# Optimization experiments

Measured on AMD Instinct MI355X. Metric: run time of the kernel, lower is better.

## Reference

```python
import jax, jax.numpy as jnp
import numpy as np

M, NQ, NKV = 8, 256, 4096
E, H, D = 1024, 16, 64  # embed_dim, num_heads, head_dim
SCALE = D ** -0.5


def setup_inputs() -> dict:
    key = jax.random.key(0)
    ks = jax.random.split(key, 6)
    zq = jax.random.normal(ks[0], (M, NQ, E), dtype=jnp.float32)
    zkv = jax.random.normal(ks[1], (M, NKV, E), dtype=jnp.float32)
    xq = jax.random.normal(ks[2], (M, NQ, E), dtype=jnp.float32)
    xkv = jax.random.normal(ks[3], (M, NKV, E), dtype=jnp.float32)
    Wq = jax.random.normal(ks[4], (E, H * D), dtype=jnp.float32) / np.sqrt(E)
    Wk = jax.random.normal(ks[5], (E, H * D), dtype=jnp.float32) / np.sqrt(E)
    raw_head_weights = jnp.ones((H,), dtype=jnp.float32)
    return {"zq": zq, "zkv": zkv, "xq": xq, "xkv": xkv,
            "Wq": Wq, "Wk": Wk, "raw_head_weights": raw_head_weights}


def reference(zq, zkv, xq, xkv, Wq, Wk, raw_head_weights):
    # project + split heads: [m, h, n, d]
    q = jnp.einsum('mne,ehd->mhnd', zq, Wq.reshape(E, H, D))
    k = jnp.einsum('mne,ehd->mhnd', zkv, Wk.reshape(E, H, D))
    # SDPA with V = xkv broadcast across heads
    scores = jnp.einsum('mhqd,mhkd->mhqk', q, k) * SCALE
    attn = jax.nn.softmax(scores, axis=-1)
    # attn @ V with broadcast V [m, nkv, dx] -> per-head outputs [m, h, nq, dx]
    out = jnp.einsum('mhqk,mkd->mhqd', attn, xkv)
    # head-weighted combine + residual
    head_weights = jax.nn.softmax(raw_head_weights, axis=0)
    xq_update = jnp.einsum('mhqd,h->mqd', out, head_weights)
    xq_out = xq + xq_update
    return (zq, xq_out)
```

## Files before the change

kernel.cpp:

```cpp
#include <hip/hip_runtime.h>
#include <hip/hip_bf16.h>
#include <stdint.h>

#define MB_  8
#define NQ_  256
#define NKV_ 4096
#define E_   1024
#define H_   16
#define D_   64

typedef __bf16 bf16x8 __attribute__((ext_vector_type(8)));
typedef float  f32x4  __attribute__((ext_vector_type(4)));
typedef unsigned short u16;
typedef unsigned short u16x8 __attribute__((ext_vector_type(8)));

#define MFMA16(a,b,c) __builtin_amdgcn_mfma_f32_16x16x32_bf16((a),(b),(c),0,0,0)

__device__ __forceinline__ u16 f2bf(float f) {
  uint32_t u = __float_as_uint(f);
  u += 0x7fffu + ((u >> 16) & 1u);
  return (u16)(u >> 16);
}

__device__ __forceinline__ void gload_lds16(const void* g, void* l) {
  __builtin_amdgcn_global_load_lds(
      (const __attribute__((address_space(1))) void*)g,
      (__attribute__((address_space(3))) void*)l, 16, 0, 0);
}

__device__ __forceinline__ void stage_tile(const char* __restrict__ g, int ldbytes,
                                           char* lds, int t) {
  int srcCB = (((t & 7) ^ ((t >> 3) & 7)) << 4);
  const char* gp = g + (long long)(t >> 3) * ldbytes + srcCB;
  char* lp = lds + ((t >> 6) << 10);
#pragma unroll
  for (int i = 0; i < 4; ++i) {
    gload_lds16(gp + (long long)(32 * i) * ldbytes, lp + i * 4096);
  }
}

__device__ __forceinline__ bf16x8 read_frag(const char* lds, int r, int cb) {
  return *(const bf16x8*)(lds + r * 128 + (cb ^ ((r & 7) << 4)));
}

template <int MODE>
__global__ __launch_bounds__(256, 2) void gemm_nt(
    const u16* __restrict__ A, const u16* __restrict__ Bt, void* __restrict__ Cv,
    int lda, int ldb, int ldc, int K,
    long long sA, long long sB, long long sC) {
  __shared__ __align__(16) char smA[16384];
  __shared__ __align__(16) char smB[16384];
  int zz = blockIdx.z;
  int b = (MODE == 2) ? (zz & 7) : zz;
  int ks = (MODE == 2) ? (zz >> 3) : 0;
  long long koff = (long long)ks * 1024;

  unsigned nwg = gridDim.x * gridDim.y;
  unsigned orig = blockIdx.y * gridDim.x + blockIdx.x;
  unsigned cpx = nwg >> 3;
  unsigned swz = (orig & 7) * cpx + (orig >> 3);
  unsigned bx = swz % gridDim.x, by = swz / gridDim.x;

  const char* Ap = (const char*)(A + (long long)b * sA + (long long)by * 128 * lda + koff);
  const char* Bp = (const char*)(Bt + (long long)b * sB + (long long)bx * 128 * ldb + koff);

  int t = threadIdx.x, lane = t & 63;
  int wm = t >> 7, wn = (t >> 6) & 1;
  int rl = lane & 15, kq = lane >> 4;

  f32x4 acc[4][4];
#pragma unroll
  for (int i = 0; i < 4; ++i)
#pragma unroll
    for (int j = 0; j < 4; ++j) acc[i][j] = (f32x4){0.f, 0.f, 0.f, 0.f};

  int ldab = lda * 2, ldbb = ldb * 2;
  for (int k0 = 0; k0 < K; k0 += 64) {
    stage_tile(Ap + k0 * 2, ldab, smA, t);
    stage_tile(Bp + k0 * 2, ldbb, smB, t);
    __syncthreads();
    bf16x8 af[4][2], bf[4][2];
#pragma unroll
    for (int f = 0; f < 4; ++f)
#pragma unroll
      for (int ksl = 0; ksl < 2; ++ksl) {
        af[f][ksl] = read_frag(smA, wm * 64 + f * 16 + rl, ksl * 64 + kq * 16);
        bf[f][ksl] = read_frag(smB, wn * 64 + f * 16 + rl, ksl * 64 + kq * 16);
      }
#pragma unroll
    for (int fm = 0; fm < 4; ++fm)
#pragma unroll
      for (int fn = 0; fn < 4; ++fn) {
        acc[fm][fn] = MFMA16(af[fm][0], bf[fn][0], acc[fm][fn]);
        acc[fm][fn] = MFMA16(af[fm][1], bf[fn][1], acc[fm][fn]);
      }
    __syncthreads();
  }

#pragma unroll
  for (int fm = 0; fm < 4; ++fm)
#pragma unroll
    for (int fn = 0; fn < 4; ++fn)
#pragma unroll
      for (int j = 0; j < 4; ++j) {
        int row = by * 128 + wm * 64 + fm * 16 + kq * 4 + j;
        int col = bx * 128 + wn * 64 + fn * 16 + rl;
        if (MODE == 0) {
          ((u16*)Cv)[(long long)b * sC + (long long)row * ldc + col] = f2bf(acc[fm][fn][j]);
        } else {
          ((float*)Cv)[((long long)(ks * 8 + b)) * sC + (long long)row * ldc + col] =
              acc[fm][fn][j];
        }
      }
}

__device__ __forceinline__ void stage32(const char* __restrict__ g, int ldbytes,
                                        char* ldsbuf, int t, long long koffB) {
  int w = t >> 6, lane = t & 63;
#pragma unroll
  for (int i = 0; i < 2; ++i) {
    int c = w + i * 8;
    int slot = c * 64 + lane;
    int row = slot >> 2, c16 = slot & 3;
    int srcc = (c16 ^ ((row >> 1) & 3)) << 4;
    gload_lds16(g + (long long)row * ldbytes + koffB + srcc,
                ldsbuf + c * 1024);
  }
}

__device__ __forceinline__ bf16x8 frag32(const char* ldsbuf, int r, int kq) {
  return *(const bf16x8*)(ldsbuf + r * 64 + ((kq ^ ((r >> 1) & 3)) << 4));
}

__global__ __launch_bounds__(512, 2) void gemm256(
    const u16* __restrict__ A, const u16* __restrict__ Bt, u16* __restrict__ C,
    int lda, int ldb, int ldc, int K) {
  extern __shared__ char lds[];

  unsigned nwg = gridDim.x * gridDim.y;
  unsigned orig = blockIdx.y * gridDim.x + blockIdx.x;
  unsigned cpx = nwg >> 3;
  unsigned swz = (orig & 7) * cpx + (orig >> 3);
  unsigned bx = swz % gridDim.x, by = swz / gridDim.x;

  const char* Ap = (const char*)(A + (long long)by * 256 * lda);
  const char* Bp = (const char*)(Bt + (long long)bx * 256 * ldb);
  int ldab = lda * 2, ldbb = ldb * 2;

  int t = threadIdx.x, lane = t & 63;
  int wid = t >> 6, wm = wid >> 2, wn = wid & 3;
  int rl = lane & 15, kq = lane >> 4;

  f32x4 acc[8][4];
#pragma unroll
  for (int i = 0; i < 8; ++i)
#pragma unroll
    for (int j = 0; j < 4; ++j) acc[i][j] = (f32x4){0.f, 0.f, 0.f, 0.f};

  stage32(Ap, ldab, lds, t, 0);
  stage32(Bp, ldbb, lds + 16384, t, 0);
  stage32(Ap, ldab, lds + 32768, t, 64);
  stage32(Bp, ldbb, lds + 32768 + 16384, t, 64);
  asm volatile("s_waitcnt vmcnt(4)" ::: "memory");
  asm volatile("s_barrier" ::: "memory");

  int NT = K >> 5;
  for (int ts = 0; ts < NT; ++ts) {
    char* bufA = lds + (ts & 3) * 32768;
    char* bufB = bufA + 16384;
    if (ts + 2 < NT) {
      char* nb = lds + ((ts + 2) & 3) * 32768;
      stage32(Ap, ldab, nb, t, (long long)(ts + 2) << 6);
      stage32(Bp, ldbb, nb + 16384, t, (long long)(ts + 2) << 6);
    }
    bf16x8 af[8], bv[4];
#pragma unroll
    for (int fr = 0; fr < 8; ++fr) af[fr] = frag32(bufA, wm * 128 + fr * 16 + rl, kq);
#pragma unroll
    for (int fc = 0; fc < 4; ++fc) bv[fc] = frag32(bufB, wn * 64 + fc * 16 + rl, kq);
    __builtin_amdgcn_s_setprio(1);
#pragma unroll
    for (int fr = 0; fr < 8; ++fr)
#pragma unroll
      for (int fc = 0; fc < 4; ++fc)
        acc[fr][fc] = MFMA16(af[fr], bv[fc], acc[fr][fc]);
    __builtin_amdgcn_s_setprio(0);
    if (ts + 2 < NT)
      asm volatile("s_waitcnt vmcnt(4)" ::: "memory");
    else
      asm volatile("s_waitcnt vmcnt(0)" ::: "memory");
    asm volatile("s_barrier" ::: "memory");
  }

#pragma unroll
  for (int fr = 0; fr < 8; ++fr)
#pragma unroll
    for (int fc = 0; fc < 4; ++fc)
#pragma unroll
      for (int j = 0; j < 4; ++j) {
        int row = by * 256 + wm * 128 + fr * 16 + kq * 4 + j;
        int col = bx * 256 + wn * 64 + fc * 16 + rl;
        C[(long long)row * ldc + col] = f2bf(acc[fr][fc][j]);
      }
}

__global__ void pv_combine_copy(const float* __restrict__ part, const float* __restrict__ xq,
                                const float* __restrict__ zq, float* __restrict__ out0,
                                float* __restrict__ out1) {
  int bid = blockIdx.x;
  if (bid < 2048) {
    int i = bid * 256 + threadIdx.x;
    ((float4*)out0)[i] = ((const float4*)zq)[i];
  } else {
    int i = (bid - 2048) * 256 + threadIdx.x;
    float4 s = ((const float4*)xq)[i];
#pragma unroll
    for (int k = 0; k < 4; ++k) {
      float4 p = ((const float4*)(part + (long long)k * 2097152))[i];
      s.x += p.x; s.y += p.y; s.z += p.z; s.w += p.w;
    }
    ((float4*)out1)[i] = s;
  }
}

__global__ __launch_bounds__(256, 4) void attn_stats(
    const u16* __restrict__ qg, const u16* __restrict__ kg,
    float* __restrict__ lstP) {
  __shared__ __align__(16) char smQ[16384];
  __shared__ __align__(16) char smK[16384];
  int kt = blockIdx.x, qt = blockIdx.y;
  int m = blockIdx.z >> 1, hh = blockIdx.z & 1;
  int t = threadIdx.x, lane = t & 63;
  int wm = t >> 7, wn = (t >> 6) & 1;
  int rl = lane & 15, kq = lane >> 4;

  const char* qbase = (const char*)(qg + ((long long)(m * NQ_ + qt * 128)) * 1024);
  const char* kbase = (const char*)(kg + ((long long)(m * NKV_ + kt * 128)) * 1024);

  for (int hi = 0; hi < 8; ++hi) {
    int h = hh * 8 + hi;
    stage_tile(qbase + h * 128, 2048, smQ, t);
    stage_tile(kbase + h * 128, 2048, smK, t);
    __syncthreads();
    bf16x8 kf[4][2], qf[4][2];
#pragma unroll
    for (int f = 0; f < 4; ++f)
#pragma unroll
      for (int ksl = 0; ksl < 2; ++ksl) {
        kf[f][ksl] = read_frag(smK, wm * 64 + f * 16 + rl, ksl * 64 + kq * 16);
        qf[f][ksl] = read_frag(smQ, wn * 64 + f * 16 + rl, ksl * 64 + kq * 16);
      }
    float rs[4] = {0.f, 0.f, 0.f, 0.f};
#pragma unroll
    for (int fm = 0; fm < 4; ++fm)
#pragma unroll
      for (int fn = 0; fn < 4; ++fn) {
        f32x4 sc = (f32x4){0.f, 0.f, 0.f, 0.f};
        sc = MFMA16(kf[fm][0], qf[fn][0], sc);
        sc = MFMA16(kf[fm][1], qf[fn][1], sc);
        rs[fn] += (__expf(sc[0]) + __expf(sc[1])) + (__expf(sc[2]) + __expf(sc[3]));
      }
#pragma unroll
    for (int fn = 0; fn < 4; ++fn) {
      float v = rs[fn];
      v += __shfl_xor(v, 16);
      v += __shfl_xor(v, 32);
      if (lane < 16) {
        int q = qt * 128 + wn * 64 + fn * 16 + rl;
        lstP[(long long)(kt * 2 + wm) * 32768 + ((m * H_ + h) << 8) + q] = v;
      }
    }
    __syncthreads();
  }
}

__global__ void stats_combine(const float* __restrict__ lp, float* __restrict__ lst) {
  int i = blockIdx.x * 256 + threadIdx.x;
  float s = 0.f;
#pragma unroll
  for (int k = 0; k < 64; ++k) s += lp[(long long)k * 32768 + i];
  lst[i] = s;
}

__global__ __launch_bounds__(256, 2) void pbar_kernel(
    const u16* __restrict__ qg, const u16* __restrict__ kg,
    const float* __restrict__ lstat,
    const float* __restrict__ rawhw, u16* __restrict__ Pbar) {
  __shared__ __align__(16) char smQ[16384];
  __shared__ __align__(16) char smK[16384];
  __shared__ float scf[2048];
  int kt = blockIdx.x, qt = blockIdx.y, m = blockIdx.z;
  int q0 = qt * 128, k0 = kt * 128;
  int t = threadIdx.x, lane = t & 63;
  int wm = t >> 7, wn = (t >> 6) & 1;
  int rl = lane & 15, kq = lane >> 4;

  float hm = -1e30f;
  for (int i = 0; i < H_; ++i) hm = fmaxf(hm, rawhw[i]);
  float hs = 0.f, hw[H_];
  for (int i = 0; i < H_; ++i) { hw[i] = __expf(rawhw[i] - hm); hs += hw[i]; }
  float hinv = 1.f / hs;
  for (int idx = t; idx < 2048; idx += 256) {
    int h = idx >> 7, r = idx & 127;
    scf[idx] = hw[h] * hinv / lstat[((m * H_ + h) << 8) + q0 + r];
  }

  f32x4 pacc[4][4];
#pragma unroll
  for (int i = 0; i < 4; ++i)
#pragma unroll
    for (int j = 0; j < 4; ++j) pacc[i][j] = (f32x4){0.f, 0.f, 0.f, 0.f};

  const char* qbase = (const char*)(qg + ((long long)(m * NQ_ + q0)) * 1024);
  const char* kbase = (const char*)(kg + ((long long)(m * NKV_ + k0)) * 1024);

  for (int h = 0; h < H_; ++h) {
    stage_tile(qbase + h * 128, 2048, smQ, t);
    stage_tile(kbase + h * 128, 2048, smK, t);
    __syncthreads();
    bf16x8 af[4][2], bfr[4][2];
#pragma unroll
    for (int f = 0; f < 4; ++f)
#pragma unroll
      for (int ksl = 0; ksl < 2; ++ksl) {
        af[f][ksl] = read_frag(smQ, wm * 64 + f * 16 + rl, ksl * 64 + kq * 16);
        bfr[f][ksl] = read_frag(smK, wn * 64 + f * 16 + rl, ksl * 64 + kq * 16);
      }
#pragma unroll
    for (int fm = 0; fm < 4; ++fm) {
      int rbase = wm * 64 + fm * 16 + kq * 4;
      float cf0 = scf[(h << 7) + rbase + 0];
      float cf1 = scf[(h << 7) + rbase + 1];
      float cf2 = scf[(h << 7) + rbase + 2];
      float cf3 = scf[(h << 7) + rbase + 3];
#pragma unroll
      for (int fn = 0; fn < 4; ++fn) {
        f32x4 sc = (f32x4){0.f, 0.f, 0.f, 0.f};
        sc = MFMA16(af[fm][0], bfr[fn][0], sc);
        sc = MFMA16(af[fm][1], bfr[fn][1], sc);
        pacc[fm][fn][0] += cf0 * __expf(sc[0]);
        pacc[fm][fn][1] += cf1 * __expf(sc[1]);
        pacc[fm][fn][2] += cf2 * __expf(sc[2]);
        pacc[fm][fn][3] += cf3 * __expf(sc[3]);
      }
    }
    __syncthreads();
  }
#pragma unroll
  for (int fm = 0; fm < 4; ++fm)
#pragma unroll
    for (int fn = 0; fn < 4; ++fn)
#pragma unroll
      for (int j = 0; j < 4; ++j) {
        int row = q0 + wm * 64 + fm * 16 + kq * 4 + j;
        int col = k0 + wn * 64 + fn * 16 + rl;
        Pbar[(((long long)m * NQ_ + row) << 12) + col] = f2bf(pacc[fm][fn][j]);
      }
}

__global__ void prep_kernel(const float* __restrict__ zq, u16* __restrict__ zqb,
                            const float* __restrict__ zkv, u16* __restrict__ zkvb,
                            const float* __restrict__ Wq, u16* __restrict__ WqT,
                            const float* __restrict__ Wk, u16* __restrict__ WkT,
                            const float* __restrict__ xkv, u16* __restrict__ xkvT) {
  __shared__ float tile[64][65];
  int bid = blockIdx.x;
  if (bid < 17408) {
    const float* in; u16* out; long long i;
    if (bid < 1024) { in = zq; out = zqb; i = (long long)bid * 256 + threadIdx.x; }
    else { in = zkv; out = zkvb; i = (long long)(bid - 1024) * 256 + threadIdx.x; }
    const float4* p = (const float4*)in + i * 2;
    float4 a = p[0], b = p[1];
    u16x8 v;
    v[0] = f2bf(a.x); v[1] = f2bf(a.y); v[2] = f2bf(a.z); v[3] = f2bf(a.w);
    v[4] = f2bf(b.x); v[5] = f2bf(b.y); v[6] = f2bf(b.z); v[7] = f2bf(b.w);
    *(u16x8*)(out + i * 8) = v;
    return;
  }
  const float* in; u16* out; int R, C; float alpha; int r0, c0;
  if (bid < 17664) {
    int id = bid - 17408;
    in = Wq; out = WqT; R = 1024; C = 1024; alpha = 0.125f;
    r0 = (id & 15) * 64; c0 = (id >> 4) * 64;
  } else if (bid < 17920) {
    int id = bid - 17664;
    in = Wk; out = WkT; R = 1024; C = 1024; alpha = 1.0f;
    r0 = (id & 15) * 64; c0 = (id >> 4) * 64;
  } else {
    int id = bid - 17920;
    int bz = id >> 10, rem = id & 1023;
    in = xkv + (long long)bz * NKV_ * E_;
    out = xkvT + (long long)bz * NKV_ * E_;
    R = NKV_; C = E_; alpha = 1.0f;
    r0 = (rem & 63) * 64; c0 = (rem >> 6) * 64;
  }
  int t = threadIdx.x;
  int rr = t >> 4, c4 = t & 15;
#pragma unroll
  for (int i = 0; i < 4; ++i) {
    float4 v = *(const float4*)(in + (long long)(r0 + rr + i * 16) * C + c0 + c4 * 4);
    float* d = &tile[rr + i * 16][c4 * 4];
    d[0] = v.x; d[1] = v.y; d[2] = v.z; d[3] = v.w;
  }
  __syncthreads();
  int cc = t >> 3, r8 = t & 7;
#pragma unroll
  for (int i = 0; i < 2; ++i) {
    int c = cc + i * 32;
    u16x8 v;
#pragma unroll
    for (int j = 0; j < 8; ++j) v[j] = f2bf(alpha * tile[r8 * 8 + j][c]);
    *(u16x8*)(out + (long long)(c0 + c) * R + r0 + r8 * 8) = v;
  }
}

extern "C" void kernel_launch(void* const* d_in, const int* in_sizes, int n_in,
                              void* d_out, int out_size, void* d_ws, size_t ws_size,
                              hipStream_t stream) {
  const float* zq  = (const float*)d_in[0];
  const float* zkv = (const float*)d_in[1];
  const float* xq  = (const float*)d_in[2];
  const float* xkv = (const float*)d_in[3];
  const float* Wq  = (const float*)d_in[4];
  const float* Wk  = (const float*)d_in[5];
  const float* rhw = (const float*)d_in[6];
  float* out = (float*)d_out;

  char* ws = (char*)d_ws;
  u16* WqT  = (u16*)(ws);
  u16* WkT  = (u16*)(ws + (2ull << 20));
  u16* zqb  = (u16*)(ws + (4ull << 20));
  u16* qb   = (u16*)(ws + (8ull << 20));
  u16* kb   = (u16*)(ws + (12ull << 20));
  u16* xkvT = (u16*)(ws + (76ull << 20));
  char* zr  = ws + (140ull << 20);
  u16* zkvb = (u16*)zr;
  u16* Pbar = (u16*)zr;
  float* lst  = (float*)(zr + (18ull << 20));
  float* lstP = (float*)(zr + (20ull << 20));
  float* pvP  = (float*)(zr + (28ull << 20));

  (void)hipFuncSetAttribute((const void*)gemm256,
                            hipFuncAttributeMaxDynamicSharedMemorySize, 131072);

  prep_kernel<<<26112, 256, 0, stream>>>(zq, zqb, zkv, zkvb, Wq, WqT, Wk, WkT, xkv, xkvT);

  gemm_nt<0><<<dim3(8, 16, 1), 256, 0, stream>>>(zqb, WqT, qb,
                                                 1024, 1024, 1024, 1024, 0, 0, 0);
  gemm256<<<dim3(4, 128, 1), 512, 131072, stream>>>(zkvb, WkT, kb, 1024, 1024, 1024, 1024);

  attn_stats<<<dim3(32, 2, 16), 256, 0, stream>>>(qb, kb, lstP);
  stats_combine<<<128, 256, 0, stream>>>(lstP, lst);

  pbar_kernel<<<dim3(32, 2, 8), 256, 0, stream>>>(qb, kb, lst, rhw, Pbar);

  gemm_nt<2><<<dim3(8, 2, 32), 256, 0, stream>>>(Pbar, xkvT, pvP,
                                                 4096, 4096, 1024, 1024,
                                                 256LL * 4096, 1024LL * 4096,
                                                 256LL * 1024);
  pv_combine_copy<<<4096, 256, 0, stream>>>(pvP, xq, zq, out,
                                            out + (long long)MB_ * NQ_ * E_);
}
```

Baseline: 300.9 us.

## Fuse zkv fp32-to-bf16 conversion into the K-projection GEMM A-operand load

The separate prep pass that converted zkv (32768x1024 fp32) to bf16 is removed. The K-projection GEMM now loads fp32 A tiles into registers, converts them to bf16 and writes swizzled LDS itself, with a register double buffer and a 2-stage LDS buffer in place of the 4-stage async-to-LDS pipeline. This drops one full write and reread of the bf16 copy of zkv. In exchange the GEMM reads A at twice the byte width, uses more VGPRs, and runs a shallower pipeline.

```diff
diff --git a/kernel.cpp b/kernel.cpp
--- a/kernel.cpp
+++ b/kernel.cpp
@@ -114,8 +114,8 @@
       }
 }
 
-__device__ __forceinline__ void stage32(const char* __restrict__ g, int ldbytes,
-                                        char* ldsbuf, int t, long long koffB) {
+__device__ __forceinline__ void stageB32(const char* __restrict__ g, int ldbytes,
+                                         char* ldsbuf, int t, long long koffB) {
   int w = t >> 6, lane = t & 63;
 #pragma unroll
   for (int i = 0; i < 2; ++i) {
@@ -123,8 +123,29 @@
     int slot = c * 64 + lane;
     int row = slot >> 2, c16 = slot & 3;
     int srcc = (c16 ^ ((row >> 1) & 3)) << 4;
-    gload_lds16(g + (long long)row * ldbytes + koffB + srcc,
-                ldsbuf + c * 1024);
+    gload_lds16(g + (long long)row * ldbytes + koffB + srcc, ldsbuf + c * 1024);
+  }
+}
+
+__device__ __forceinline__ void loadA32(const float* __restrict__ Apf, int lda,
+                                        int t, int k0, float4 r[4]) {
+  int row = t >> 1, kh = (t & 1) * 16;
+  const float* p = Apf + (long long)row * lda + k0 + kh;
+#pragma unroll
+  for (int i = 0; i < 4; ++i) r[i] = *(const float4*)(p + i * 4);
+}
+
+__device__ __forceinline__ void writeA32(char* bufA, int t, const float4 r[4]) {
+  int row = t >> 1, kh = t & 1;
+  int sw = (row >> 1) & 3;
+#pragma unroll
+  for (int i = 0; i < 2; ++i) {
+    float4 a = r[i * 2], b = r[i * 2 + 1];
+    u16x8 v;
+    v[0] = f2bf(a.x); v[1] = f2bf(a.y); v[2] = f2bf(a.z); v[3] = f2bf(a.w);
+    v[4] = f2bf(b.x); v[5] = f2bf(b.y); v[6] = f2bf(b.z); v[7] = f2bf(b.w);
+    int c16 = kh * 2 + i;
+    *(u16x8*)(bufA + row * 64 + ((c16 ^ sw) << 4)) = v;
   }
 }
 
@@ -132,8 +153,8 @@
   return *(const bf16x8*)(ldsbuf + r * 64 + ((kq ^ ((r >> 1) & 3)) << 4));
 }
 
-__global__ __launch_bounds__(512, 2) void gemm256(
-    const u16* __restrict__ A, const u16* __restrict__ Bt, u16* __restrict__ C,
+__global__ __launch_bounds__(512, 2) void gemm256f(
+    const float* __restrict__ A, const u16* __restrict__ Bt, u16* __restrict__ C,
     int lda, int ldb, int ldc, int K) {
   extern __shared__ char lds[];
 
@@ -143,52 +164,91 @@
   unsigned swz = (orig & 7) * cpx + (orig >> 3);
   unsigned bx = swz % gridDim.x, by = swz / gridDim.x;
 
-  const char* Ap = (const char*)(A + (long long)by * 256 * lda);
+  const float* Apf = A + (long long)by * 256 * lda;
   const char* Bp = (const char*)(Bt + (long long)bx * 256 * ldb);
-  int ldab = lda * 2, ldbb = ldb * 2;
+  int ldbb = ldb * 2;
 
   int t = threadIdx.x, lane = t & 63;
   int wid = t >> 6, wm = wid >> 2, wn = wid & 3;
   int rl = lane & 15, kq = lane >> 4;
 
+  char* bufA0 = lds;
+  char* bufA1 = lds + 16384;
+  char* bufB0 = lds + 32768;
+  char* bufB1 = lds + 49152;
+
   f32x4 acc[8][4];
 #pragma unroll
   for (int i = 0; i < 8; ++i)
 #pragma unroll
     for (int j = 0; j < 4; ++j) acc[i][j] = (f32x4){0.f, 0.f, 0.f, 0.f};
 
-  stage32(Ap, ldab, lds, t, 0);
-  stage32(Bp, ldbb, lds + 16384, t, 0);
-  stage32(Ap, ldab, lds + 32768, t, 64);
-  stage32(Bp, ldbb, lds + 32768 + 16384, t, 64);
-  asm volatile("s_waitcnt vmcnt(4)" ::: "memory");
+  float4 rEven[4], rOdd[4];
+
+  stageB32(Bp, ldbb, bufB0, t, 0);
+  __builtin_amdgcn_sched_barrier(0);
+  loadA32(Apf, lda, t, 0, rEven);
+  loadA32(Apf, lda, t, 32, rOdd);
+  asm volatile("s_waitcnt vmcnt(0)" ::: "memory");
+  writeA32(bufA0, t, rEven);
+  asm volatile("s_waitcnt lgkmcnt(0)" ::: "memory");
   asm volatile("s_barrier" ::: "memory");
 
   int NT = K >> 5;
-  for (int ts = 0; ts < NT; ++ts) {
-    char* bufA = lds + (ts & 3) * 32768;
-    char* bufB = bufA + 16384;
+  for (int ts = 0; ts < NT; ts += 2) {
+    if (ts + 1 < NT) stageB32(Bp, ldbb, bufB1, t, (long long)(ts + 1) << 6);
+    __builtin_amdgcn_sched_barrier(0);
+    if (ts + 2 < NT) loadA32(Apf, lda, t, (ts + 2) << 5, rEven);
+    {
+      bf16x8 af[8], bv[4];
+#pragma unroll
+      for (int fr = 0; fr < 8; ++fr) af[fr] = frag32(bufA0, wm * 128 + fr * 16 + rl, kq);
+#pragma unroll
+      for (int fc = 0; fc < 4; ++fc) bv[fc] = frag32(bufB0, wn * 64 + fc * 16 + rl, kq);
+      __builtin_amdgcn_s_setprio(1);
+#pragma unroll
+      for (int fr = 0; fr < 8; ++fr)
+#pragma unroll
+        for (int fc = 0; fc < 4; ++fc)
+          acc[fr][fc] = MFMA16(af[fr], bv[fc], acc[fr][fc]);
+      __builtin_amdgcn_s_setprio(0);
+    }
+    if (ts + 1 < NT) {
+      if (ts + 2 < NT)
+        asm volatile("s_waitcnt vmcnt(4)" ::: "memory");
+      else
+        asm volatile("s_waitcnt vmcnt(0)" ::: "memory");
+      writeA32(bufA1, t, rOdd);
+      asm volatile("s_waitcnt lgkmcnt(0)" ::: "memory");
+    }
+    asm volatile("s_barrier" ::: "memory");
+    if (ts + 1 >= NT) break;
+
+    if (ts + 2 < NT) stageB32(Bp, ldbb, bufB0, t, (long long)(ts + 2) << 6);
+    __builtin_amdgcn_sched_barrier(0);
+    if (ts + 3 < NT) loadA32(Apf, lda, t, (ts + 3) << 5, rOdd);
+    {
+      bf16x8 af[8], bv[4];
+#pragma unroll
+      for (int fr = 0; fr < 8; ++fr) af[fr] = frag32(bufA1, wm * 128 + fr * 16 + rl, kq);
+#pragma unroll
+      for (int fc = 0; fc < 4; ++fc) bv[fc] = frag32(bufB1, wn * 64 + fc * 16 + rl, kq);
+      __builtin_amdgcn_s_setprio(1);
+#pragma unroll
+      for (int fr = 0; fr < 8; ++fr)
+#pragma unroll
+        for (int fc = 0; fc < 4; ++fc)
+          acc[fr][fc] = MFMA16(af[fr], bv[fc], acc[fr][fc]);
+      __builtin_amdgcn_s_setprio(0);
+    }
     if (ts + 2 < NT) {
-      char* nb = lds + ((ts + 2) & 3) * 32768;
-      stage32(Ap, ldab, nb, t, (long long)(ts + 2) << 6);
-      stage32(Bp, ldbb, nb + 16384, t, (long long)(ts + 2) << 6);
-    }
-    bf16x8 af[8], bv[4];
-#pragma unroll
-    for (int fr = 0; fr < 8; ++fr) af[fr] = frag32(bufA, wm * 128 + fr * 16 + rl, kq);
-#pragma unroll
-    for (int fc = 0; fc < 4; ++fc) bv[fc] = frag32(bufB, wn * 64 + fc * 16 + rl, kq);
-    __builtin_amdgcn_s_setprio(1);
-#pragma unroll
-    for (int fr = 0; fr < 8; ++fr)
-#pragma unroll
-      for (int fc = 0; fc < 4; ++fc)
-        acc[fr][fc] = MFMA16(af[fr], bv[fc], acc[fr][fc]);
-    __builtin_amdgcn_s_setprio(0);
-    if (ts + 2 < NT)
-      asm volatile("s_waitcnt vmcnt(4)" ::: "memory");
-    else
-      asm volatile("s_waitcnt vmcnt(0)" ::: "memory");
+      if (ts + 3 < NT)
+        asm volatile("s_waitcnt vmcnt(4)" ::: "memory");
+      else
+        asm volatile("s_waitcnt vmcnt(0)" ::: "memory");
+      writeA32(bufA0, t, rEven);
+      asm volatile("s_waitcnt lgkmcnt(0)" ::: "memory");
+    }
     asm volatile("s_barrier" ::: "memory");
   }
 
@@ -359,35 +419,32 @@
 }
 
 __global__ void prep_kernel(const float* __restrict__ zq, u16* __restrict__ zqb,
-                            const float* __restrict__ zkv, u16* __restrict__ zkvb,
                             const float* __restrict__ Wq, u16* __restrict__ WqT,
                             const float* __restrict__ Wk, u16* __restrict__ WkT,
                             const float* __restrict__ xkv, u16* __restrict__ xkvT) {
   __shared__ float tile[64][65];
   int bid = blockIdx.x;
-  if (bid < 17408) {
-    const float* in; u16* out; long long i;
-    if (bid < 1024) { in = zq; out = zqb; i = (long long)bid * 256 + threadIdx.x; }
-    else { in = zkv; out = zkvb; i = (long long)(bid - 1024) * 256 + threadIdx.x; }
-    const float4* p = (const float4*)in + i * 2;
+  if (bid < 1024) {
+    long long i = (long long)bid * 256 + threadIdx.x;
+    const float4* p = (const float4*)zq + i * 2;
     float4 a = p[0], b = p[1];
     u16x8 v;
     v[0] = f2bf(a.x); v[1] = f2bf(a.y); v[2] = f2bf(a.z); v[3] = f2bf(a.w);
     v[4] = f2bf(b.x); v[5] = f2bf(b.y); v[6] = f2bf(b.z); v[7] = f2bf(b.w);
-    *(u16x8*)(out + i * 8) = v;
+    *(u16x8*)(zqb + i * 8) = v;
     return;
   }
   const float* in; u16* out; int R, C; float alpha; int r0, c0;
-  if (bid < 17664) {
-    int id = bid - 17408;
+  if (bid < 1280) {
+    int id = bid - 1024;
     in = Wq; out = WqT; R = 1024; C = 1024; alpha = 0.125f;
     r0 = (id & 15) * 64; c0 = (id >> 4) * 64;
-  } else if (bid < 17920) {
-    int id = bid - 17664;
+  } else if (bid < 1536) {
+    int id = bid - 1280;
     in = Wk; out = WkT; R = 1024; C = 1024; alpha = 1.0f;
     r0 = (id & 15) * 64; c0 = (id >> 4) * 64;
   } else {
-    int id = bid - 17920;
+    int id = bid - 1536;
     int bz = id >> 10, rem = id & 1023;
     in = xkv + (long long)bz * NKV_ * E_;
     out = xkvT + (long long)bz * NKV_ * E_;
@@ -434,20 +491,19 @@
   u16* kb   = (u16*)(ws + (12ull << 20));
   u16* xkvT = (u16*)(ws + (76ull << 20));
   char* zr  = ws + (140ull << 20);
-  u16* zkvb = (u16*)zr;
   u16* Pbar = (u16*)zr;
   float* lst  = (float*)(zr + (18ull << 20));
   float* lstP = (float*)(zr + (20ull << 20));
   float* pvP  = (float*)(zr + (28ull << 20));
 
-  (void)hipFuncSetAttribute((const void*)gemm256,
-                            hipFuncAttributeMaxDynamicSharedMemorySize, 131072);
-
-  prep_kernel<<<26112, 256, 0, stream>>>(zq, zqb, zkv, zkvb, Wq, WqT, Wk, WkT, xkv, xkvT);
+  (void)hipFuncSetAttribute((const void*)gemm256f,
+                            hipFuncAttributeMaxDynamicSharedMemorySize, 65536);
+
+  prep_kernel<<<9728, 256, 0, stream>>>(zq, zqb, Wq, WqT, Wk, WkT, xkv, xkvT);
 
   gemm_nt<0><<<dim3(8, 16, 1), 256, 0, stream>>>(zqb, WqT, qb,
                                                  1024, 1024, 1024, 1024, 0, 0, 0);
-  gemm256<<<dim3(4, 128, 1), 512, 131072, stream>>>(zkvb, WkT, kb, 1024, 1024, 1024, 1024);
+  gemm256f<<<dim3(4, 128, 1), 512, 65536, stream>>>(zkv, WkT, kb, 1024, 1024, 1024, 1024);
 
   attn_stats<<<dim3(32, 2, 16), 256, 0, stream>>>(qb, kb, lstP);
   stats_combine<<<128, 256, 0, stream>>>(lstP, lst);
```

Measured after the change: 303.2 us. About the same (+0.8%).
